# Optimization experiments

Measured on AMD Instinct MI355X. Metric: run time of the kernel, lower is better.

The kernel has to match this reference:

```python
import jax, jax.numpy as jnp
import numpy as np

N = 50000
LEAKY_SLOPE = 0.2


def gat_layer(x, src, dst, W, a_src, a_dst, bias, concat):
    """PyG-style GATConv (eval mode, self-loops already in src/dst).
    x: [N, Fin]; W: [Fin, H*C]; a_src, a_dst: [H, C]; bias: [H*C] or [C].
    """
    H, C = a_src.shape
    h = (x @ W).reshape(-1, H, C)                      # [N, H, C]
    alpha_src = jnp.einsum('nhc,hc->nh', h, a_src)      # [N, H]
    alpha_dst = jnp.einsum('nhc,hc->nh', h, a_dst)      # [N, H]
    e = jax.nn.leaky_relu(alpha_src[src] + alpha_dst[dst], LEAKY_SLOPE)  # [E, H]
    # scatter-softmax over incoming edges of each destination node
    m = jax.lax.stop_gradient(jax.ops.segment_max(e, dst, num_segments=N))
    e = jnp.exp(e - m[dst])
    denom = jax.ops.segment_sum(e, dst, num_segments=N)  # [N, H]
    alpha = e / (denom[dst] + 1e-16)                     # [E, H]
    msg = h[src] * alpha[:, :, None]                     # [E, H, C]
    out = jax.ops.segment_sum(msg, dst, num_segments=N)  # [N, H, C]
    out = out.reshape(-1, H * C) if concat else out.mean(axis=1)
    return out + bias


def setup_inputs() -> dict:
    key = jax.random.key(0)
    ks = jax.random.split(key, 10)
    Fin, Hd, Hh = 256, 64, 4
    E = 1600000
    x = jax.random.normal(ks[0], (N, Fin), dtype=jnp.float32)
    edge_index = jax.random.randint(ks[1], (2, E), 0, N, dtype=jnp.int64)
    s = 1.0 / np.sqrt(Fin)
    W1 = jax.random.normal(ks[2], (Fin, Hh * Hd), dtype=jnp.float32) * s
    att_src1 = jax.random.normal(ks[3], (Hh, Hd), dtype=jnp.float32) * (1.0 / np.sqrt(Hd))
    att_dst1 = jax.random.normal(ks[4], (Hh, Hd), dtype=jnp.float32) * (1.0 / np.sqrt(Hd))
    b1 = jnp.zeros((Hh * Hd,), dtype=jnp.float32)
    W2 = jax.random.normal(ks[5], (Hh * Hd, Hd), dtype=jnp.float32) * (1.0 / np.sqrt(Hh * Hd))
    att_src2 = jax.random.normal(ks[6], (1, Hd), dtype=jnp.float32) * (1.0 / np.sqrt(Hd))
    att_dst2 = jax.random.normal(ks[7], (1, Hd), dtype=jnp.float32) * (1.0 / np.sqrt(Hd))
    b2 = jnp.zeros((Hd,), dtype=jnp.float32)
    return {"x": x, "edge_index": edge_index, "W1": W1, "att_src1": att_src1,
            "att_dst1": att_dst1, "b1": b1, "W2": W2, "att_src2": att_src2,
            "att_dst2": att_dst2, "b2": b2}


def reference(x, edge_index, W1, att_src1, att_dst1, b1, W2, att_src2, att_dst2, b2):
    # PyG GATConv adds self-loops by default
    loop = jnp.arange(N, dtype=edge_index.dtype)
    src = jnp.concatenate([edge_index[0], loop])
    dst = jnp.concatenate([edge_index[1], loop])
    h = gat_layer(x, src, dst, W1, att_src1, att_dst1, b1, concat=True)
    h = jax.nn.elu(h)            # dropout is identity in eval mode
    out = gat_layer(h, src, dst, W2, att_src2, att_dst2, b2, concat=False)
    return out
```

## Files before the change

### kernel.cpp

```cpp
#include <hip/hip_runtime.h>


typedef __attribute__((ext_vector_type(8))) short short8;
typedef __attribute__((ext_vector_type(4))) float floatx4;
typedef __attribute__((ext_vector_type(2))) float fx2;
typedef __attribute__((ext_vector_type(4))) unsigned int uintx4;

#define FIN 256
#define H1 4
#define CH 64
#define CAP 16384
#define G2S 40

__device__ __forceinline__ float bf2f(ushort u) {
    union { unsigned int i; float f; } v; v.i = ((unsigned int)u) << 16; return v.f;
}
__device__ __forceinline__ ushort f2bf(float f) {
    union { float f; unsigned int i; } v; v.f = f;
    unsigned int r = v.i + 0x7fffu + ((v.i >> 16) & 1u);
    return (ushort)(r >> 16);
}
__device__ __forceinline__ float load_in(const void* p, int i, int f) {
    return f ? ((const float*)p)[i] : bf2f(((const ushort*)p)[i]);
}
__device__ __forceinline__ int load_idx(const void* p, long long i, int f64) {
    return f64 ? (int)((const long long*)p)[i] : ((const int*)p)[i];
}

__device__ __forceinline__ int pk_off(int row, int k, int KT) {
    return (((row >> 4) * KT + (k >> 5)) << 9) + (((k >> 3) & 3) << 7) +
           ((row & 15) << 3) + (k & 7);
}
__device__ __forceinline__ void pk_dec(int po0, int& row, int& k) {
    int tile = po0 >> 9;
    row = ((tile >> 3) << 4) + ((po0 >> 3) & 15);
    k = ((tile & 7) << 5) + (((po0 >> 7) & 3) << 3);
}

__device__ __forceinline__ float edge_p(float s) {
    s = fmaxf(s, 0.2f * s);
    return __expf(s);
}

__device__ __forceinline__ void accum16(fx2* acc, uint4 v0, uint4 v1,
                                        float p, float& l) {
    l += p;
    fx2 pv = {p, p};
    unsigned w[8] = {v0.x, v0.y, v0.z, v0.w, v1.x, v1.y, v1.z, v1.w};
#pragma unroll
    for (int u = 0; u < 8; ++u) {
        union { unsigned i; float fl; } lo, hi;
        lo.i = w[u] << 16; hi.i = w[u] & 0xffff0000u;
        fx2 c = {lo.fl, hi.fl};
        acc[u] += pv * c;
    }
}

__device__ __forceinline__ void accum8(fx2* acc, uint4 v, float p, float& l) {
    l += p;
    fx2 pv = {p, p};
    unsigned w[4] = {v.x, v.y, v.z, v.w};
#pragma unroll
    for (int u = 0; u < 4; ++u) {
        union { unsigned i; float fl; } lo, hi;
        lo.i = w[u] << 16; hi.i = w[u] & 0xffff0000u;
        fx2 c = {lo.fl, hi.fl};
        acc[u] += pv * c;
    }
}

__global__ __launch_bounds__(256) void probe_kernel(const uint4* __restrict__ x4,
                                                    const uint4* __restrict__ ei4,
                                                    int* __restrict__ flags,
                                                    int* __restrict__ bcnt) {
    __shared__ int s_nan, s_odd;
    int t = threadIdx.x;
    bcnt[t] = 0;
    if (t == 0) { s_nan = 0; s_odd = 0; }
    __syncthreads();
    int nanc = 0, oddc = 0;
#pragma unroll
    for (int j = 0; j < 4; ++j) {
        uint4 v = x4[t * 4 + j];
        unsigned w[4] = {v.x, v.y, v.z, v.w};
#pragma unroll
        for (int u = 0; u < 4; ++u) {
            if (((w[u] >> 7) & 0xFFu) == 0xFFu) nanc++;
            if (((w[u] >> 23) & 0xFFu) == 0xFFu) nanc++;
        }
    }
#pragma unroll
    for (int j = 0; j < 4; ++j) {
        uint4 v = ei4[t * 4 + j];
        if (v.y != 0u) oddc++;
        if (v.w != 0u) oddc++;
    }
    if (nanc) atomicAdd(&s_nan, nanc);
    if (oddc) atomicAdd(&s_odd, oddc);
    __syncthreads();
    if (t == 0) {
        flags[0] = (s_nan >= 2) ? 1 : 0;
        flags[1] = (s_odd == 0) ? 1 : 0;
    }
}

__global__ __launch_bounds__(256) void prep_bucket_kernel(
        const void* __restrict__ x, const void* __restrict__ W1,
        const void* __restrict__ W2, ushort* __restrict__ xb,
        ushort* __restrict__ Wt1, ushort* __restrict__ Wt2,
        const void* __restrict__ ei, int* __restrict__ bcnt,
        unsigned int* __restrict__ buckets,
        int E, int Etot, int Nn, const int* __restrict__ flags,
        int PB_conv, int PB_tr_end) {
    __shared__ int lcnt[256], lbase[256], lcur[256];
    int bid = blockIdx.x, t = threadIdx.x;
    int f = flags[0];
    if (bid < PB_conv) {
        if (!f) return;
        int po0 = bid * 2048 + t * 8;
        int row, k0; pk_dec(po0, row, k0);
        int si = row * FIN + k0;
        float4 v0 = ((const float4*)x)[si / 4];
        float4 v1 = ((const float4*)x)[si / 4 + 1];
        ushort4 o0, o1;
        o0.x = f2bf(v0.x); o0.y = f2bf(v0.y); o0.z = f2bf(v0.z); o0.w = f2bf(v0.w);
        o1.x = f2bf(v1.x); o1.y = f2bf(v1.y); o1.z = f2bf(v1.z); o1.w = f2bf(v1.w);
        *(ushort4*)(xb + po0) = o0;
        *(ushort4*)(xb + po0 + 4) = o1;
        return;
    }
    if (bid < PB_tr_end) {
        int j = (bid - PB_conv) * 256 + t;
        if (j < (FIN * FIN) / 8) {
            int po0 = j * 8;
            int n, k0; pk_dec(po0, n, k0);
            ushort4 o0, o1;
            o0.x = f2bf(load_in(W1, (k0 + 0) * FIN + n, f));
            o0.y = f2bf(load_in(W1, (k0 + 1) * FIN + n, f));
            o0.z = f2bf(load_in(W1, (k0 + 2) * FIN + n, f));
            o0.w = f2bf(load_in(W1, (k0 + 3) * FIN + n, f));
            o1.x = f2bf(load_in(W1, (k0 + 4) * FIN + n, f));
            o1.y = f2bf(load_in(W1, (k0 + 5) * FIN + n, f));
            o1.z = f2bf(load_in(W1, (k0 + 6) * FIN + n, f));
            o1.w = f2bf(load_in(W1, (k0 + 7) * FIN + n, f));
            *(ushort4*)(Wt1 + po0) = o0;
            *(ushort4*)(Wt1 + po0 + 4) = o1;
        } else {
            int po0 = (j - (FIN * FIN) / 8) * 8;
            int n, k0; pk_dec(po0, n, k0);
            ushort4 o0, o1;
            o0.x = f2bf(load_in(W2, (k0 + 0) * CH + n, f));
            o0.y = f2bf(load_in(W2, (k0 + 1) * CH + n, f));
            o0.z = f2bf(load_in(W2, (k0 + 2) * CH + n, f));
            o0.w = f2bf(load_in(W2, (k0 + 3) * CH + n, f));
            o1.x = f2bf(load_in(W2, (k0 + 4) * CH + n, f));
            o1.y = f2bf(load_in(W2, (k0 + 5) * CH + n, f));
            o1.z = f2bf(load_in(W2, (k0 + 6) * CH + n, f));
            o1.w = f2bf(load_in(W2, (k0 + 7) * CH + n, f));
            *(ushort4*)(Wt2 + po0) = o0;
            *(ushort4*)(Wt2 + po0 + 4) = o1;
        }
        return;
    }
    lcnt[t] = 0; lcur[t] = 0;
    __syncthreads();
    int f64 = flags[1];
    int base = (bid - PB_tr_end) * 4096 + t;
    unsigned int val[16]; int bk[16]; bool ok[16];
#pragma unroll
    for (int j = 0; j < 16; ++j) {
        int e = base + j * 256;
        ok[j] = e < Etot;
        bk[j] = 0; val[j] = 0;
        if (ok[j]) {
            int s, d;
            if (e < E) {
                s = load_idx(ei, e, f64);
                d = load_idx(ei, (long long)E + e, f64);
            } else {
                s = d = e - E;
            }
            s = min(max(s, 0), Nn - 1);
            d = min(max(d, 0), Nn - 1);
            bk[j] = d >> 8;
            val[j] = ((unsigned int)s << 8) | (unsigned int)(d & 255);
            atomicAdd(&lcnt[bk[j]], 1);
        }
    }
    __syncthreads();
    if (lcnt[t] > 0) lbase[t] = atomicAdd(&bcnt[t], lcnt[t]);
    __syncthreads();
#pragma unroll
    for (int j = 0; j < 16; ++j) {
        if (ok[j]) {
            int p = lbase[bk[j]] + atomicAdd(&lcur[bk[j]], 1);
            if (p < CAP) buckets[(size_t)bk[j] * CAP + p] = val[j];
        }
    }
}

__device__ __forceinline__ void gemm_core(const ushort* __restrict__ Axb,
                                          const ushort* __restrict__ Xraw,
                                          ushort* __restrict__ Asub,
                                          const ushort* __restrict__ Bt,
                                          ushort* __restrict__ C,
                                          int M,
                                          const void* __restrict__ aS,
                                          const void* __restrict__ aD,
                                          float* __restrict__ alphaS,
                                          float* __restrict__ alphaD,
                                          int f, int gx, int head) {
    const int KT = FIN >> 5;
    int tid = threadIdx.x;
    int wave = tid >> 6, lane = tid & 63, quad = lane >> 4, l16 = lane & 15;
    int rbase = gx * 256 + wave * 64;
    int cbase = head * 64;
    int lsub = (quad << 7) + (l16 << 3);
    floatx4 acc[4][4];
#pragma unroll
    for (int i = 0; i < 4; i++)
#pragma unroll
        for (int j = 0; j < 4; j++) acc[i][j] = (floatx4)0.f;

    if (f) {
#pragma unroll 2
        for (int kb = 0; kb < FIN; kb += 32) {
            int kt = kb >> 5;
            short8 a[4], b[4];
#pragma unroll
            for (int mt = 0; mt < 4; mt++) {
                int tr = (rbase + mt * 16) >> 4;
                a[mt] = *reinterpret_cast<const short8*>(
                    Axb + (((size_t)(tr * KT + kt)) << 9) + lsub);
            }
#pragma unroll
            for (int nt = 0; nt < 4; nt++) {
                int tc = (cbase + nt * 16) >> 4;
                b[nt] = *reinterpret_cast<const short8*>(
                    Bt + (((size_t)(tc * KT + kt)) << 9) + lsub);
            }
#pragma unroll
            for (int mt = 0; mt < 4; mt++)
#pragma unroll
                for (int nt = 0; nt < 4; nt++)
                    acc[mt][nt] = __builtin_amdgcn_mfma_f32_16x16x32_bf16(
                        a[mt], b[nt], acc[mt][nt], 0, 0, 0);
        }
    } else {
        int chunk = tid & 3, rr = tid >> 2;
        for (int kb = 0; kb < FIN; kb += 32) {
            __syncthreads();
#pragma unroll
            for (int rd = 0; rd < 4; ++rd) {
                int row = gx * 256 + rd * 64 + rr;
                if (row >= M) row = M - 1;
                uint4 v = *(const uint4*)(Xraw + (size_t)row * FIN + kb + chunk * 8);
                *(uint4*)(Asub + (rd * 64 + rr) * G2S + chunk * 8) = v;
            }
            __syncthreads();
            int kt = kb >> 5;
            short8 b[4];
#pragma unroll
            for (int nt = 0; nt < 4; nt++) {
                int tc = (cbase + nt * 16) >> 4;
                b[nt] = *reinterpret_cast<const short8*>(
                    Bt + (((size_t)(tc * KT + kt)) << 9) + lsub);
            }
#pragma unroll
            for (int mt = 0; mt < 4; mt++) {
                short8 a = *reinterpret_cast<const short8*>(
                    Asub + (wave * 64 + mt * 16 + l16) * G2S + quad * 8);
#pragma unroll
                for (int nt = 0; nt < 4; nt++)
                    acc[mt][nt] = __builtin_amdgcn_mfma_f32_16x16x32_bf16(
                        a, b[nt], acc[mt][nt], 0, 0, 0);
            }
        }
    }
    float asv[4], adv[4];
#pragma unroll
    for (int nt = 0; nt < 4; nt++) {
        int col = cbase + nt * 16 + l16;
        asv[nt] = load_in(aS, col, f);
        adv[nt] = load_in(aD, col, f);
    }
#pragma unroll
    for (int mt = 0; mt < 4; mt++) {
#pragma unroll
        for (int r = 0; r < 4; r++) {
            int row = rbase + mt * 16 + quad * 4 + r;
            float ps = 0.f, pd = 0.f;
#pragma unroll
            for (int nt = 0; nt < 4; nt++) {
                float w = acc[mt][nt][r];
                ps += w * asv[nt];
                pd += w * adv[nt];
            }
#pragma unroll
            for (int off = 8; off > 0; off >>= 1) {
                ps += __shfl_xor(ps, off, 16);
                pd += __shfl_xor(pd, off, 16);
            }
            if (row < M) {
                if (l16 == 0) {
                    alphaS[row * H1 + head] = ps;
                    alphaD[row * H1 + head] = pd;
                }
#pragma unroll
                for (int nt = 0; nt < 4; nt++) {
                    int col = cbase + nt * 16 + l16;
                    size_t caddr = ((size_t)(col >> 7) * M + row) * 128 + (col & 127);
                    C[caddr] = f2bf(acc[mt][nt][r]);
                }
            }
        }
    }
}

__global__ __launch_bounds__(256) void gemm1_pass2_kernel(
        const ushort* __restrict__ Axb, const ushort* __restrict__ Xraw,
        const ushort* __restrict__ Bt,
        ushort* __restrict__ C, int M,
        const void* __restrict__ aS, const void* __restrict__ aD,
        float* __restrict__ alphaS, float* __restrict__ alphaD,
        const int* __restrict__ flags, int NB, int nbx,
        const int* __restrict__ bcnt, const unsigned int* __restrict__ buckets,
        int* __restrict__ offs, int* __restrict__ csr_src, int Nn) {
    __shared__ int part[256], sc[256], sc4[4][256];
    __shared__ ushort Asub[256 * G2S];
    int bid = blockIdx.x;
    int t = threadIdx.x;
    if (bid >= NB) {
        int gg = bid - NB;
        int r = (gg & 7) | ((gg >> 5) << 3);
        int h = (gg >> 3) & 3;
        if (r < nbx)
            gemm_core(Axb, Xraw, Asub, Bt, C, M, aS, aD, alphaS, alphaD,
                      flags[0], r, h);
        return;
    }
    int b = bid;
    int w = t >> 6;
    part[t] = bcnt[t];
    sc4[0][t] = 0; sc4[1][t] = 0; sc4[2][t] = 0; sc4[3][t] = 0;
    __syncthreads();
#pragma unroll
    for (int off = 1; off < 256; off <<= 1) {
        int v = (t >= off) ? part[t - off] : 0;
        __syncthreads();
        part[t] += v;
        __syncthreads();
    }
    int basepos = (b == 0) ? 0 : part[b - 1];
    int nEdges = min(bcnt[b], CAP);
    const unsigned int* bk = buckets + (size_t)b * CAP;
    for (int i = t; i < nEdges; i += 256)
        atomicAdd(&sc4[w][bk[i] & 255], 1);
    __syncthreads();
    int c0 = sc4[0][t], c1 = sc4[1][t], c2 = sc4[2][t], c3 = sc4[3][t];
    int mycount = c0 + c1 + c2 + c3;
    sc[t] = mycount;
    __syncthreads();
#pragma unroll
    for (int off = 1; off < 256; off <<= 1) {
        int v = (t >= off) ? sc[t - off] : 0;
        __syncthreads();
        sc[t] += v;
        __syncthreads();
    }
    int excl = sc[t] - mycount;
    int gnode = b * 256 + t;
    if (gnode <= Nn) offs[gnode] = basepos + excl;
    sc4[0][t] = excl;
    sc4[1][t] = excl + c0;
    sc4[2][t] = excl + c0 + c1;
    sc4[3][t] = excl + c0 + c1 + c2;
    __syncthreads();
    for (int i = t; i < nEdges; i += 256) {
        unsigned int v = bk[i];
        int p = atomicAdd(&sc4[w][v & 255], 1);
        csr_src[basepos + p] = (int)(v >> 8);
    }
}

__global__ __launch_bounds__(256) void gemm2_kernel(const ushort* __restrict__ A,
                                                    const ushort* __restrict__ Bt,
                                                    ushort* __restrict__ C,
                                                    int M,
                                                    const void* __restrict__ aS,
                                                    const void* __restrict__ aD,
                                                    float* __restrict__ alphaS,
                                                    float* __restrict__ alphaD,
                                                    const int* __restrict__ flags) {
    __shared__ ushort Asub[256 * G2S];
    const int KT = FIN >> 5;
    int t = threadIdx.x;
    int f = flags[0];
    int wave = t >> 6, lane = t & 63, quad = lane >> 4, l16 = lane & 15;
    int rbase = blockIdx.x * 256 + wave * 64;
    int lsub = (quad << 7) + (l16 << 3);
    int chunk = t & 3, rr = t >> 2;
    floatx4 acc[4][4];
#pragma unroll
    for (int i = 0; i < 4; i++)
#pragma unroll
        for (int j = 0; j < 4; j++) acc[i][j] = (floatx4)0.f;

    for (int kb = 0; kb < FIN; kb += 32) {
        __syncthreads();
#pragma unroll
        for (int rd = 0; rd < 4; ++rd) {
            int row = blockIdx.x * 256 + rd * 64 + rr;
            if (row >= M) row = M - 1;
            uint4 v = *(const uint4*)(A + (size_t)row * FIN + kb + chunk * 8);
            *(uint4*)(Asub + (rd * 64 + rr) * G2S + chunk * 8) = v;
        }
        __syncthreads();
        int kt = kb >> 5;
        short8 b[4];
#pragma unroll
        for (int nt = 0; nt < 4; nt++) {
            b[nt] = *reinterpret_cast<const short8*>(
                Bt + (((size_t)(nt * KT + kt)) << 9) + lsub);
        }
#pragma unroll
        for (int mt = 0; mt < 4; mt++) {
            short8 a = *reinterpret_cast<const short8*>(
                Asub + (wave * 64 + mt * 16 + l16) * G2S + quad * 8);
#pragma unroll
            for (int nt = 0; nt < 4; nt++)
                acc[mt][nt] = __builtin_amdgcn_mfma_f32_16x16x32_bf16(
                    a, b[nt], acc[mt][nt], 0, 0, 0);
        }
    }
    float asv[4], adv[4];
#pragma unroll
    for (int nt = 0; nt < 4; nt++) {
        int col = nt * 16 + l16;
        asv[nt] = load_in(aS, col, f);
        adv[nt] = load_in(aD, col, f);
    }
#pragma unroll
    for (int mt = 0; mt < 4; mt++) {
#pragma unroll
        for (int r = 0; r < 4; r++) {
            int row = rbase + mt * 16 + quad * 4 + r;
            float ps = 0.f, pd = 0.f;
#pragma unroll
            for (int nt = 0; nt < 4; nt++) {
                float w = acc[mt][nt][r];
                ps += w * asv[nt];
                pd += w * adv[nt];
            }
#pragma unroll
            for (int off = 8; off > 0; off >>= 1) {
                ps += __shfl_xor(ps, off, 16);
                pd += __shfl_xor(pd, off, 16);
            }
            if (row < M) {
                if (l16 == 0) {
                    alphaS[row] = ps;
                    alphaD[row] = pd;
                }
#pragma unroll
                for (int nt = 0; nt < 4; nt++) {
                    int col = nt * 16 + l16;
                    C[(size_t)row * CH + col] = f2bf(acc[mt][nt][r]);
                }
            }
        }
    }
}

__global__ __launch_bounds__(256) void gat_node1_pass(
        const int* __restrict__ csr_src, const int* __restrict__ offs,
        const float* __restrict__ asrc, const float* __restrict__ adst,
        const ushort* __restrict__ h1p, const void* __restrict__ b1,
        ushort* __restrict__ hmidb, int Nn, const int* __restrict__ flags,
        int plane) {
    int f = flags[0];
    int wave = threadIdx.x >> 6, lane = threadIdx.x & 63;
    int n = blockIdx.x * 4 + wave;
    if (n >= Nn) return;
    int slot = lane >> 3, cg = lane & 7;
    int head = plane * 2 + (cg >> 2);
    float ad = adst[n * H1 + head];
    unsigned rowbase = (unsigned)(plane * Nn) * 128u + (unsigned)cg * 16u;
    int beg = offs[n], end = offs[n + 1];
    fx2 acc[8];
#pragma unroll
    for (int u = 0; u < 8; ++u) acc[u] = (fx2)0.f;
    float l = 0.f;

    int e = beg;
    while (e + 16 <= end) {
        int sa = csr_src[e + slot];
        int sb = csr_src[e + 8 + slot];
        float aa = asrc[sa * H1 + head];
        float ab = asrc[sb * H1 + head];
        const uint4* ra = (const uint4*)(h1p + rowbase + (unsigned)sa * 128u);
        const uint4* rb = (const uint4*)(h1p + rowbase + (unsigned)sb * 128u);
        uint4 va0 = ra[0], va1 = ra[1];
        uint4 vb0 = rb[0], vb1 = rb[1];
        float pa = edge_p(aa + ad);
        float pb = edge_p(ab + ad);
        accum16(acc, va0, va1, pa, l);
        accum16(acc, vb0, vb1, pb, l);
        e += 16;
    }
    if (e < end) {
        int ea = e + slot, eb = e + 8 + slot;
        bool oka = ea < end, okb = eb < end;
        int sa = csr_src[oka ? ea : beg];
        int sb = csr_src[okb ? eb : beg];
        float aa = asrc[sa * H1 + head];
        float ab = asrc[sb * H1 + head];
        const uint4* ra = (const uint4*)(h1p + rowbase + (unsigned)sa * 128u);
        const uint4* rb = (const uint4*)(h1p + rowbase + (unsigned)sb * 128u);
        uint4 va0 = ra[0], va1 = ra[1];
        uint4 vb0 = rb[0], vb1 = rb[1];
        float pa = edge_p(oka ? aa + ad : -1e30f);
        float pb = edge_p(okb ? ab + ad : -1e30f);
        accum16(acc, va0, va1, pa, l);
        accum16(acc, vb0, vb1, pb, l);
    }
#pragma unroll
    for (int off = 8; off <= 32; off <<= 1) {
#pragma unroll
        for (int u = 0; u < 8; ++u) {
            acc[u][0] += __shfl_xor(acc[u][0], off);
            acc[u][1] += __shfl_xor(acc[u][1], off);
        }
        l += __shfl_xor(l, off);
    }
    if (slot == 0) {
        float inv = 1.f / (l + 1e-16f);
        int cb = plane * 128 + cg * 16;
        unsigned ow[8];
#pragma unroll
        for (int u = 0; u < 8; ++u) {
            float o0 = acc[u][0] * inv + load_in(b1, cb + 2 * u, f);
            float o1 = acc[u][1] * inv + load_in(b1, cb + 2 * u + 1, f);
            o0 = o0 > 0.f ? o0 : __expf(o0) - 1.f;
            o1 = o1 > 0.f ? o1 : __expf(o1) - 1.f;
            ow[u] = (unsigned)f2bf(o0) | ((unsigned)f2bf(o1) << 16);
        }
        uintx4 st0 = {ow[0], ow[1], ow[2], ow[3]};
        uintx4 st1 = {ow[4], ow[5], ow[6], ow[7]};
        uintx4* dst = (uintx4*)(hmidb + (size_t)n * 256 + cb);
        __builtin_nontemporal_store(st0, dst);
        __builtin_nontemporal_store(st1, dst + 1);
    }
}

__global__ __launch_bounds__(256) void gat_node2(const int* __restrict__ csr_src,
                                                 const int* __restrict__ offs,
                                                 const float* __restrict__ asrc,
                                                 const float* __restrict__ adst,
                                                 const ushort* __restrict__ h2b,
                                                 const void* __restrict__ b2,
                                                 void* __restrict__ out, int Nn,
                                                 const int* __restrict__ flags) {
    int f = flags[0];
    int wave = threadIdx.x >> 6, lane = threadIdx.x & 63;
    int n = blockIdx.x * 4 + wave;
    if (n >= Nn) return;
    int slot = lane >> 3, cg = lane & 7;
    float ad = adst[n];
    unsigned rowoff = (unsigned)cg * 8u;
    int beg = offs[n], end = offs[n + 1];
    fx2 acc[4];
#pragma unroll
    for (int u = 0; u < 4; ++u) acc[u] = (fx2)0.f;
    float l = 0.f;

    int e = beg;
    while (e + 16 <= end) {
        int sa = csr_src[e + slot];
        int sb = csr_src[e + 8 + slot];
        float aa = asrc[sa];
        float ab = asrc[sb];
        uint4 va = *(const uint4*)(h2b + rowoff + (unsigned)sa * 64u);
        uint4 vb = *(const uint4*)(h2b + rowoff + (unsigned)sb * 64u);
        float pa = edge_p(aa + ad);
        float pb = edge_p(ab + ad);
        accum8(acc, va, pa, l);
        accum8(acc, vb, pb, l);
        e += 16;
    }
    if (e < end) {
        int ea = e + slot, eb = e + 8 + slot;
        bool oka = ea < end, okb = eb < end;
        int sa = csr_src[oka ? ea : beg];
        int sb = csr_src[okb ? eb : beg];
        float aa = asrc[sa];
        float ab = asrc[sb];
        uint4 va = *(const uint4*)(h2b + rowoff + (unsigned)sa * 64u);
        uint4 vb = *(const uint4*)(h2b + rowoff + (unsigned)sb * 64u);
        float pa = edge_p(oka ? aa + ad : -1e30f);
        float pb = edge_p(okb ? ab + ad : -1e30f);
        accum8(acc, va, pa, l);
        accum8(acc, vb, pb, l);
    }
#pragma unroll
    for (int off = 8; off <= 32; off <<= 1) {
#pragma unroll
        for (int u = 0; u < 4; ++u) {
            acc[u][0] += __shfl_xor(acc[u][0], off);
            acc[u][1] += __shfl_xor(acc[u][1], off);
        }
        l += __shfl_xor(l, off);
    }
    if (slot == 0) {
        float inv = 1.f / (l + 1e-16f);
        float o[8];
#pragma unroll
        for (int u = 0; u < 4; ++u) {
            o[2 * u]     = acc[u][0] * inv + load_in(b2, cg * 8 + 2 * u, f);
            o[2 * u + 1] = acc[u][1] * inv + load_in(b2, cg * 8 + 2 * u + 1, f);
        }
        if (f) {
            float* op = (float*)out + (unsigned)n * 64u + (unsigned)cg * 8u;
            floatx4 s0 = {o[0], o[1], o[2], o[3]};
            floatx4 s1 = {o[4], o[5], o[6], o[7]};
            __builtin_nontemporal_store(s0, (floatx4*)op);
            __builtin_nontemporal_store(s1, (floatx4*)(op + 4));
        } else {
            uintx4 st = {(unsigned)f2bf(o[0]) | ((unsigned)f2bf(o[1]) << 16),
                         (unsigned)f2bf(o[2]) | ((unsigned)f2bf(o[3]) << 16),
                         (unsigned)f2bf(o[4]) | ((unsigned)f2bf(o[5]) << 16),
                         (unsigned)f2bf(o[6]) | ((unsigned)f2bf(o[7]) << 16)};
            __builtin_nontemporal_store(st,
                (uintx4*)((ushort*)out + (unsigned)n * 64u + (unsigned)cg * 8u));
        }
    }
}

extern "C" void kernel_launch(void* const* d_in, const int* in_sizes, int n_in,
                              void* d_out, int out_size, void* d_ws, size_t ws_size,
                              hipStream_t stream) {
    const void* x   = d_in[0];
    const void* ei  = d_in[1];
    const void* W1  = d_in[2];
    const void* as1 = d_in[3];
    const void* ad1 = d_in[4];
    const void* b1  = d_in[5];
    const void* W2  = d_in[6];
    const void* as2 = d_in[7];
    const void* ad2 = d_in[8];
    const void* b2  = d_in[9];

    const int Nn = in_sizes[0] / FIN;
    const int E  = in_sizes[1] / 2;
    const int ET = E + Nn;
    const int NB = (Nn + 255) >> 8;

    char* ws = (char*)d_ws;
    size_t off = 0;
    auto alloc = [&](size_t bytes) {
        size_t o = off;
        off += (bytes + 255) & ~(size_t)255;
        return o;
    };
    ushort* xb    = (ushort*)(ws + alloc((size_t)Nn * FIN * 2));
    ushort* h1b   = (ushort*)(ws + alloc((size_t)Nn * FIN * 2));
    ushort* hmidb = (ushort*)(ws + alloc((size_t)Nn * FIN * 2));
    ushort* h2b   = (ushort*)(ws + alloc((size_t)Nn * CH * 2));
    ushort* Wt1   = (ushort*)(ws + alloc((size_t)FIN * FIN * 2));
    ushort* Wt2   = (ushort*)(ws + alloc((size_t)CH * FIN * 2));
    float* as1f   = (float*)(ws + alloc((size_t)Nn * H1 * 4));
    float* ad1f   = (float*)(ws + alloc((size_t)Nn * H1 * 4));
    float* as2f   = (float*)(ws + alloc((size_t)Nn * 4));
    float* ad2f   = (float*)(ws + alloc((size_t)Nn * 4));
    int*   offs   = (int*)(ws + alloc((size_t)(Nn + 1) * 4));
    int*   csr    = (int*)(ws + alloc((size_t)ET * 4));
    unsigned int* buckets = (unsigned int*)(ws + alloc((size_t)256 * CAP * 4));
    int*   bcnt   = (int*)(ws + alloc(256 * 4));
    int*   flags  = (int*)(ws + alloc(256));
    (void)ws_size; (void)n_in; (void)out_size;

    probe_kernel<<<1, 256, 0, stream>>>((const uint4*)x, (const uint4*)ei, flags, bcnt);

    int PB_conv = (Nn * FIN) / 2048;
    int PB_tr   = (FIN * FIN + CH * FIN) / 2048;
    int PB_bkt  = (ET + 4095) / 4096;
    prep_bucket_kernel<<<PB_conv + PB_tr + PB_bkt, 256, 0, stream>>>(
        x, W1, W2, xb, Wt1, Wt2, ei, bcnt, buckets,
        E, ET, Nn, flags, PB_conv, PB_conv + PB_tr);

    int nbx = (Nn + 255) / 256;
    int ngrp = (nbx + 7) >> 3;
    gemm1_pass2_kernel<<<NB + ngrp * 32, 256, 0, stream>>>(
        xb, (const ushort*)x, Wt1, h1b, Nn, as1, ad1, as1f, ad1f,
        flags, NB, nbx, bcnt, buckets, offs, csr, Nn);

    gat_node1_pass<<<(Nn + 3) / 4, 256, 0, stream>>>(
        csr, offs, as1f, ad1f, h1b, b1, hmidb, Nn, flags, 0);
    gat_node1_pass<<<(Nn + 3) / 4, 256, 0, stream>>>(
        csr, offs, as1f, ad1f, h1b, b1, hmidb, Nn, flags, 1);

    gemm2_kernel<<<(Nn + 255) / 256, 256, 0, stream>>>(
        hmidb, Wt2, h2b, Nn, as2, ad2, as2f, ad2f, flags);
    gat_node2<<<(Nn + 3) / 4, 256, 0, stream>>>(csr, offs, as2f, ad2f, h2b, b2, d_out, Nn, flags);
}
```

Baseline: 335.5 us.

## Double-buffer GEMM A tiles in LDS and use nontemporal stores for outputs

The two LDS-staged GEMM paths (layer-1 fallback and layer-2) now double-buffer their A tiles. The next K slice is loaded into the alternate buffer while MFMAs run on the current one, and one barrier per iteration is dropped. Separately, bucket, CSR offset/source and GEMM output writes become nontemporal stores to reduce cache pollution. LDS use per block doubles, which may lower occupancy, especially in the fused pass2 kernel that also holds scan arrays.

```diff
diff --git a/kernel.cpp b/kernel.cpp
--- a/kernel.cpp
+++ b/kernel.cpp
@@ -194,7 +194,9 @@
     for (int j = 0; j < 16; ++j) {
         if (ok[j]) {
             int p = lbase[bk[j]] + atomicAdd(&lcur[bk[j]], 1);
-            if (p < CAP) buckets[(size_t)bk[j] * CAP + p] = val[j];
+            if (p < CAP)
+                __builtin_nontemporal_store(val[j],
+                    buckets + (size_t)bk[j] * CAP + p);
         }
     }
 }
@@ -248,17 +250,27 @@
         }
     } else {
         int chunk = tid & 3, rr = tid >> 2;
-        for (int kb = 0; kb < FIN; kb += 32) {
+#pragma unroll
+        for (int rd = 0; rd < 4; ++rd) {
+            int row = gx * 256 + rd * 64 + rr;
+            if (row >= M) row = M - 1;
+            uint4 v = *(const uint4*)(Xraw + (size_t)row * FIN + chunk * 8);
+            *(uint4*)(Asub + (rd * 64 + rr) * G2S + chunk * 8) = v;
+        }
+        int cur = 0;
+        for (int kt = 0; kt < 8; ++kt) {
             __syncthreads();
-#pragma unroll
-            for (int rd = 0; rd < 4; ++rd) {
-                int row = gx * 256 + rd * 64 + rr;
-                if (row >= M) row = M - 1;
-                uint4 v = *(const uint4*)(Xraw + (size_t)row * FIN + kb + chunk * 8);
-                *(uint4*)(Asub + (rd * 64 + rr) * G2S + chunk * 8) = v;
-            }
-            __syncthreads();
-            int kt = kb >> 5;
+            if (kt + 1 < 8) {
+                int kb2 = (kt + 1) << 5;
+#pragma unroll
+                for (int rd = 0; rd < 4; ++rd) {
+                    int row = gx * 256 + rd * 64 + rr;
+                    if (row >= M) row = M - 1;
+                    uint4 v = *(const uint4*)(Xraw + (size_t)row * FIN + kb2 + chunk * 8);
+                    *(uint4*)(Asub + (cur ^ 1) * (256 * G2S)
+                              + (rd * 64 + rr) * G2S + chunk * 8) = v;
+                }
+            }
             short8 b[4];
 #pragma unroll
             for (int nt = 0; nt < 4; nt++) {
@@ -266,15 +278,17 @@
                 b[nt] = *reinterpret_cast<const short8*>(
                     Bt + (((size_t)(tc * KT + kt)) << 9) + lsub);
             }
+            const ushort* Ac = Asub + cur * (256 * G2S);
 #pragma unroll
             for (int mt = 0; mt < 4; mt++) {
                 short8 a = *reinterpret_cast<const short8*>(
-                    Asub + (wave * 64 + mt * 16 + l16) * G2S + quad * 8);
+                    Ac + (wave * 64 + mt * 16 + l16) * G2S + quad * 8);
 #pragma unroll
                 for (int nt = 0; nt < 4; nt++)
                     acc[mt][nt] = __builtin_amdgcn_mfma_f32_16x16x32_bf16(
                         a, b[nt], acc[mt][nt], 0, 0, 0);
             }
+            cur ^= 1;
         }
     }
     float asv[4], adv[4];
@@ -310,7 +324,7 @@
                 for (int nt = 0; nt < 4; nt++) {
                     int col = cbase + nt * 16 + l16;
                     size_t caddr = ((size_t)(col >> 7) * M + row) * 128 + (col & 127);
-                    C[caddr] = f2bf(acc[mt][nt][r]);
+                    __builtin_nontemporal_store(f2bf(acc[mt][nt][r]), C + caddr);
                 }
             }
         }
@@ -327,7 +341,7 @@
         const int* __restrict__ bcnt, const unsigned int* __restrict__ buckets,
         int* __restrict__ offs, int* __restrict__ csr_src, int Nn) {
     __shared__ int part[256], sc[256], sc4[4][256];
-    __shared__ ushort Asub[256 * G2S];
+    __shared__ ushort Asub[2 * 256 * G2S];
     int bid = blockIdx.x;
     int t = threadIdx.x;
     if (bid >= NB) {
@@ -370,7 +384,8 @@
     }
     int excl = sc[t] - mycount;
     int gnode = b * 256 + t;
-    if (gnode <= Nn) offs[gnode] = basepos + excl;
+    if (gnode <= Nn)
+        __builtin_nontemporal_store(basepos + excl, offs + gnode);
     sc4[0][t] = excl;
     sc4[1][t] = excl + c0;
     sc4[2][t] = excl + c0 + c1;
@@ -379,7 +394,7 @@
     for (int i = t; i < nEdges; i += 256) {
         unsigned int v = bk[i];
         int p = atomicAdd(&sc4[w][v & 255], 1);
-        csr_src[basepos + p] = (int)(v >> 8);
+        __builtin_nontemporal_store((int)(v >> 8), csr_src + basepos + p);
     }
 }
 
@@ -392,7 +407,7 @@
                                                     float* __restrict__ alphaS,
                                                     float* __restrict__ alphaD,
                                                     const int* __restrict__ flags) {
-    __shared__ ushort Asub[256 * G2S];
+    __shared__ ushort Asub[2 * 256 * G2S];
     const int KT = FIN >> 5;
     int t = threadIdx.x;
     int f = flags[0];
@@ -406,32 +421,44 @@
 #pragma unroll
         for (int j = 0; j < 4; j++) acc[i][j] = (floatx4)0.f;
 
-    for (int kb = 0; kb < FIN; kb += 32) {
+#pragma unroll
+    for (int rd = 0; rd < 4; ++rd) {
+        int row = blockIdx.x * 256 + rd * 64 + rr;
+        if (row >= M) row = M - 1;
+        uint4 v = *(const uint4*)(A + (size_t)row * FIN + chunk * 8);
+        *(uint4*)(Asub + (rd * 64 + rr) * G2S + chunk * 8) = v;
+    }
+    int cur = 0;
+    for (int kt = 0; kt < 8; ++kt) {
         __syncthreads();
-#pragma unroll
-        for (int rd = 0; rd < 4; ++rd) {
-            int row = blockIdx.x * 256 + rd * 64 + rr;
-            if (row >= M) row = M - 1;
-            uint4 v = *(const uint4*)(A + (size_t)row * FIN + kb + chunk * 8);
-            *(uint4*)(Asub + (rd * 64 + rr) * G2S + chunk * 8) = v;
-        }
-        __syncthreads();
-        int kt = kb >> 5;
+        if (kt + 1 < 8) {
+            int kb2 = (kt + 1) << 5;
+#pragma unroll
+            for (int rd = 0; rd < 4; ++rd) {
+                int row = blockIdx.x * 256 + rd * 64 + rr;
+                if (row >= M) row = M - 1;
+                uint4 v = *(const uint4*)(A + (size_t)row * FIN + kb2 + chunk * 8);
+                *(uint4*)(Asub + (cur ^ 1) * (256 * G2S)
+                          + (rd * 64 + rr) * G2S + chunk * 8) = v;
+            }
+        }
         short8 b[4];
 #pragma unroll
         for (int nt = 0; nt < 4; nt++) {
             b[nt] = *reinterpret_cast<const short8*>(
                 Bt + (((size_t)(nt * KT + kt)) << 9) + lsub);
         }
+        const ushort* Ac = Asub + cur * (256 * G2S);
 #pragma unroll
         for (int mt = 0; mt < 4; mt++) {
             short8 a = *reinterpret_cast<const short8*>(
-                Asub + (wave * 64 + mt * 16 + l16) * G2S + quad * 8);
+                Ac + (wave * 64 + mt * 16 + l16) * G2S + quad * 8);
 #pragma unroll
             for (int nt = 0; nt < 4; nt++)
                 acc[mt][nt] = __builtin_amdgcn_mfma_f32_16x16x32_bf16(
                     a, b[nt], acc[mt][nt], 0, 0, 0);
         }
+        cur ^= 1;
     }
     float asv[4], adv[4];
 #pragma unroll
@@ -465,7 +492,8 @@
 #pragma unroll
                 for (int nt = 0; nt < 4; nt++) {
                     int col = nt * 16 + l16;
-                    C[(size_t)row * CH + col] = f2bf(acc[mt][nt][r]);
+                    __builtin_nontemporal_store(f2bf(acc[mt][nt][r]),
+                                                C + (size_t)row * CH + col);
                 }
             }
         }
```

Measured after the change: 416.9 us. +24.3%, slower.
